# Performance work log

Measured on AMD Instinct MI355X. Metric: run time of the kernel, lower is better.

## Reference

```python
import jax, jax.numpy as jnp
import numpy as np
from jax import lax

B, D, L = 32, 256, 4096
Q, H, T = D // 4, D // 2, 3 * D // 4


def setup_inputs() -> dict:
    key = jax.random.key(0)
    ks = iter(jax.random.split(key, 64))

    def nrm(shape, s=0.02):
        return jax.random.normal(next(ks), shape, jnp.float32) * s

    inp = {"x": jax.random.normal(next(ks), (B, D, L), jnp.float32)}

    def pw(name, o, c):  # pointwise conv: weight [O,C], bias [O]
        inp[name + "_w"] = nrm((o, c))
        inp[name + "_b"] = jnp.zeros((o,), jnp.float32)

    def dw(name, c, k):  # depthwise conv: weight [C,1,K], bias [C]
        inp[name + "_w"] = nrm((c, 1, k))
        inp[name + "_b"] = jnp.zeros((c,), jnp.float32)

    inp["ln1_w"] = jnp.ones((D,), jnp.float32); inp["ln1_b"] = jnp.zeros((D,), jnp.float32)
    pw("a1p", Q, Q); dw("a1d", Q, 7)
    pw("v1", Q, Q); pw("v11", Q, Q); pw("v12", Q, Q)
    dw("c31", Q, 3)
    inp["ln2_w"] = jnp.ones((H,), jnp.float32); inp["ln2_b"] = jnp.zeros((H,), jnp.float32)
    pw("a2p", H, H); dw("a2d", H, 9)
    pw("v2", H, H); pw("v21", H, H); pw("v22", Q, Q)
    pw("p2", Q, H)
    dw("c32", Q, 3)
    inp["ln3_w"] = jnp.ones((T,), jnp.float32); inp["ln3_b"] = jnp.zeros((T,), jnp.float32)
    pw("a3p", T, T); dw("a3d", T, 11)
    pw("v3", T, T); pw("v31", T, T); pw("v32", Q, Q)
    pw("p3", Q, T)
    dw("c33", Q, 3)
    return inp


def _ln_cf(x, w, b, eps=1e-6):
    # channels_first LayerNorm: normalize over channel dim (axis=1)
    u = jnp.mean(x, axis=1, keepdims=True)
    s = jnp.mean((x - u) ** 2, axis=1, keepdims=True)
    return w[:, None] * (x - u) / jnp.sqrt(s + eps) + b[:, None]


def _pw(x, w, b):
    # 1x1 conv1d: x [B,C,L], w [O,C] -> [B,O,L]
    return jnp.einsum('bcl,oc->bol', x, w) + b[:, None]


def _dw(x, w, b, pad):
    # depthwise conv1d: x [B,C,L], w [C,1,K]
    y = lax.conv_general_dilated(x, w, (1,), [(pad, pad)],
                                 dimension_numbers=('NCH', 'OIH', 'NCH'),
                                 feature_group_count=x.shape[1])
    return y + b[:, None]


def reference(x, ln1_w, ln1_b, a1p_w, a1p_b, a1d_w, a1d_b, v1_w, v1_b,
              v11_w, v11_b, v12_w, v12_b, c31_w, c31_b,
              ln2_w, ln2_b, a2p_w, a2p_b, a2d_w, a2d_b, v2_w, v2_b,
              v21_w, v21_b, v22_w, v22_b, p2_w, p2_b, c32_w, c32_b,
              ln3_w, ln3_b, a3p_w, a3p_b, a3d_w, a3d_b, v3_w, v3_b,
              v31_w, v31_b, v32_w, v32_b, p3_w, p3_b, c33_w, c33_b):
    x = _ln_cf(x, ln1_w, ln1_b)
    xs = jnp.split(x, 4, axis=1)  # 4 chunks of Q channels

    # stage 1
    a = _dw(jax.nn.gelu(_pw(xs[0], a1p_w, a1p_b), approximate=False), a1d_w, a1d_b, 3)
    mul = _pw(a * _pw(xs[0], v1_w, v1_b), v11_w, v11_b)
    x1 = _dw(_pw(xs[1], v12_w, v12_b), c31_w, c31_b, 1) + a
    x1 = jnp.concatenate([x1, mul], axis=1)  # [B,H,L]

    # stage 2
    x1 = _ln_cf(x1, ln2_w, ln2_b)
    a = _dw(jax.nn.gelu(_pw(x1, a2p_w, a2p_b), approximate=False), a2d_w, a2d_b, 4)
    mul = _pw(a * _pw(x1, v2_w, v2_b), v21_w, v21_b)
    x2 = _dw(_pw(xs[2], v22_w, v22_b), c32_w, c32_b, 1) + _pw(a, p2_w, p2_b)
    x2 = jnp.concatenate([x2, mul], axis=1)  # [B,T,L]

    # stage 3
    x2 = _ln_cf(x2, ln3_w, ln3_b)
    a = _dw(jax.nn.gelu(_pw(x2, a3p_w, a3p_b), approximate=False), a3d_w, a3d_b, 5)
    mul = _pw(a * _pw(x2, v3_w, v3_b), v31_w, v31_b)
    x3 = _dw(_pw(xs[3], v32_w, v32_b), c33_w, c33_b, 1) + _pw(a, p3_w, p3_b)
    return jnp.concatenate([x3, mul], axis=1)  # [B,D,L]
```

## Files before the change

kernel.cpp:

```cpp
#include <hip/hip_runtime.h>
#include <cmath>


using u16 = unsigned short;
typedef short shrt8 __attribute__((ext_vector_type(8)));
typedef short shrt4 __attribute__((ext_vector_type(4)));
typedef float f32x4 __attribute__((ext_vector_type(4)));

#define DEVI __device__ __forceinline__

static constexpr int TL   = 64;
static constexpr int EXT  = 88;
static constexpr int RS   = 72;
static constexpr int SLOT = EXT * RS;
static constexpr int NW   = 8;

DEVI u16 f2bf(float f) {
    unsigned u = __float_as_uint(f);
    u += 0x7FFFu + ((u >> 16) & 1u);
    return (u16)(u >> 16);
}
DEVI float bf2f(u16 h) { return __uint_as_float(((unsigned)h) << 16); }

DEVI float gelu_f(float x) {
    const float y  = x * 0.70710678118654752f;
    const float ay = fabsf(y);
    const float t  = __builtin_amdgcn_rcpf(fmaf(0.3275911f, ay, 1.0f));
    float p = 1.061405429f;
    p = fmaf(p, t, -1.453152027f);
    p = fmaf(p, t,  1.421413741f);
    p = fmaf(p, t, -0.284496736f);
    p = fmaf(p, t,  0.254829592f);
    float er = 1.0f - p * t * __expf(-ay * ay);
    er = copysignf(er, y);
    return 0.5f * x * (1.0f + er);
}

struct SL { int a, b, c; };
DEVI int slotOf(SL s, int ch) { return ch < 64 ? s.a : (ch < 128 ? s.b : s.c); }

template<int O, int C, bool GELU, bool TOG, bool INPL>
DEVI void pw_mfma(u16* sh, SL in, SL out, const u16* Wb, const float* bias,
                  int elo, int ehi, int l0,
                  float* outg = nullptr, int bidx = 0, int ochan = 0) {
    constexpr int MR = O / 64;
    constexpr int KT = C / 32;
    constexpr int NT = 3;
    const int lane = threadIdx.x & 63;
    const int wv   = threadIdx.x >> 6;
    const int mw = wv >> 1, nw = wv & 1;
    const int col  = lane & 15;
    const int quad = lane >> 4;
    const int mrow = mw * (MR * 16) + col;
    const int kq   = quad * 8;
    const int crow = mw * (MR * 16) + quad * 4;

    f32x4 acc[MR][NT];
    #pragma unroll
    for (int mi = 0; mi < MR; ++mi) {
        const f32x4 bv = *(const f32x4*)(bias + crow + mi * 16);
        #pragma unroll
        for (int ni = 0; ni < NT; ++ni) acc[mi][ni] = bv;
    }
    bool act[NT]; int bpos[NT];
    #pragma unroll
    for (int ni = 0; ni < NT; ++ni) {
        const int nt = nw * NT + ni;
        act[ni] = (nt * 16 < ehi) && (nt * 16 + 16 > elo);
        int p = nt * 16 + col; if (p > EXT - 1) p = EXT - 1;
        bpos[ni] = p;
    }
    #pragma unroll
    for (int kt = 0; kt < KT; ++kt) {
        shrt8 af[MR];
        #pragma unroll
        for (int mi = 0; mi < MR; ++mi)
            af[mi] = *(const shrt8*)(Wb + (size_t)(mrow + mi * 16) * C + kt * 32 + kq);
        const int k0 = kt * 32;
        const u16* bs = sh + slotOf(in, k0) * SLOT + ((k0 & 63) + kq);
        #pragma unroll
        for (int ni = 0; ni < NT; ++ni) {
            if (!act[ni]) continue;
            const shrt8 bf = *(const shrt8*)(bs + bpos[ni] * RS);
            #pragma unroll
            for (int mi = 0; mi < MR; ++mi)
                acc[mi][ni] = __builtin_amdgcn_mfma_f32_16x16x32_bf16(af[mi], bf, acc[mi][ni], 0, 0, 0);
        }
    }
    if (INPL) __syncthreads();
    #pragma unroll
    for (int ni = 0; ni < NT; ++ni) {
        if (!act[ni]) continue;
        const int e = (nw * NT + ni) * 16 + col;
        if (e < elo || e >= ehi) continue;
        const int l = l0 + e;
        #pragma unroll
        for (int mi = 0; mi < MR; ++mi) {
            f32x4 v = acc[mi][ni];
            if (GELU) { v[0]=gelu_f(v[0]); v[1]=gelu_f(v[1]); v[2]=gelu_f(v[2]); v[3]=gelu_f(v[3]); }
            const int ch = crow + mi * 16;
            if (TOG) {
                float* og = outg + ((size_t)bidx * 256 + ochan + ch) * 4096 + l;
                og[0] = v[0]; og[4096] = v[1]; og[2*4096] = v[2]; og[3*4096] = v[3];
            } else {
                const bool gv = (unsigned)l < 4096u;
                shrt4 pk;
                pk[0] = gv ? (short)f2bf(v[0]) : (short)0;
                pk[1] = gv ? (short)f2bf(v[1]) : (short)0;
                pk[2] = gv ? (short)f2bf(v[2]) : (short)0;
                pk[3] = gv ? (short)f2bf(v[3]) : (short)0;
                *(shrt4*)(sh + slotOf(out, ch) * SLOT + e * RS + (ch & 63)) = pk;
            }
        }
    }
}

template<int C, int K, int PAD, int WIN, bool INPL>
DEVI void dw_mul(u16* sh, SL g, SL ao, SL v, const float* W, const float* bias,
                 int elo, int ehi) {
    const int lane = threadIdx.x & 63;
    const int wv   = threadIdx.x >> 6;
    const int nwin  = (ehi - elo + WIN - 1) / WIN;
    const int tasks = (C / 64) * nwin;
    const bool have = wv < tasks;
    float r[K + WIN - 1];
    float wk[K];
    float bo = 0.f;
    int c = 0, e0 = 0;
    if (have) {
        const int cb = wv / nwin, wi = wv - cb * nwin;
        c = cb * 64 + lane;
        #pragma unroll
        for (int k = 0; k < K; ++k) wk[k] = W[c * K + k];
        bo = bias[c];
        e0 = elo + wi * WIN;
        const u16* si = sh + slotOf(g, c) * SLOT + lane;
        #pragma unroll
        for (int m = 0; m < K + WIN - 1; ++m) {
            int e = e0 - PAD + m; if (e > EXT - 1) e = EXT - 1;
            r[m] = bf2f(si[e * RS]);
        }
    }
    if (INPL) __syncthreads();
    if (have) {
        u16* sa = sh + slotOf(ao, c) * SLOT + lane;
        u16* sv = sh + slotOf(v, c) * SLOT + lane;
        #pragma unroll
        for (int j = 0; j < WIN; ++j) {
            const int e = e0 + j;
            if (e >= ehi) break;
            float acc = bo;
            #pragma unroll
            for (int k = 0; k < K; ++k) acc = fmaf(wk[k], r[j + k], acc);
            sa[e * RS] = f2bf(acc);
            sv[e * RS] = f2bf(acc * bf2f(sv[e * RS]));
        }
    }
}

template<int C, int K, int PAD, bool ADD>
DEVI void dw_ph(u16* sh, SL in, SL add, SL out, const float* W, const float* bias,
                int elo, int ehi, int l0) {
    const int lane = threadIdx.x & 63;
    const int wv   = threadIdx.x >> 6;
    const int nwin = (ehi - elo + 7) >> 3;
    const int tasks = (C / 64) * nwin;
    for (int t = wv; t < tasks; t += NW) {
        const int cb = t / nwin, wi = t - cb * nwin;
        const int c = cb * 64 + lane;
        float wk[K];
        #pragma unroll
        for (int k = 0; k < K; ++k) wk[k] = W[c * K + k];
        const float bo = bias[c];
        const int e0 = elo + wi * 8;
        const u16* si = sh + slotOf(in, c) * SLOT + lane;
        const u16* sa = ADD ? (sh + slotOf(add, c) * SLOT + lane) : nullptr;
        u16* so = sh + slotOf(out, c) * SLOT + lane;
        float r[K + 7];
        #pragma unroll
        for (int m = 0; m < K + 7; ++m) {
            int e = e0 - PAD + m; if (e > EXT - 1) e = EXT - 1;
            r[m] = bf2f(si[e * RS]);
        }
        #pragma unroll
        for (int j = 0; j < 8; ++j) {
            const int e = e0 + j;
            if (e >= ehi) break;
            float acc = bo;
            #pragma unroll
            for (int k = 0; k < K; ++k) acc = fmaf(wk[k], r[j + k], acc);
            if (ADD) acc += bf2f(sa[e * RS]);
            const bool gv = (unsigned)(l0 + e) < 4096u;
            so[e * RS] = gv ? f2bf(acc) : (u16)0;
        }
    }
}

template<int C>
DEVI void ln_ph(u16* sh, SL s, const float* W, const float* B,
                int elo, int ehi, int l0, float* scr, float* mean, float* rstd) {
    constexpr int P = C / 64;
    const int tid = threadIdx.x;
    const int nP = ehi - elo;
    if (tid < nP * P) {
        const int e = elo + tid / P;
        const int part = tid - (tid / P) * P;
        const u16* row = sh + slotOf(s, part * 64) * SLOT + e * RS;
        float sm = 0.f, sq = 0.f;
        #pragma unroll
        for (int j = 0; j < 8; ++j) {
            shrt8 v = *(const shrt8*)(row + j * 8);
            #pragma unroll
            for (int i = 0; i < 8; ++i) { float f = bf2f((u16)v[i]); sm += f; sq += f * f; }
        }
        scr[tid * 2] = sm; scr[tid * 2 + 1] = sq;
    }
    __syncthreads();
    if (tid < nP) {
        float sm = 0.f, sq = 0.f;
        for (int p = 0; p < P; ++p) { sm += scr[(tid * P + p) * 2]; sq += scr[(tid * P + p) * 2 + 1]; }
        const float mu = sm * (1.0f / C);
        const float va = sq * (1.0f / C) - mu * mu;
        mean[elo + tid] = mu; rstd[elo + tid] = rsqrtf(va + 1e-6f);
    }
    __syncthreads();
    const int nC8 = C / 8, total = nP * nC8;
    for (int t = tid; t < total; t += 512) {
        const int e  = elo + t / nC8;
        const int c0 = (t - (t / nC8) * nC8) * 8;
        const float mu = mean[e], rs = rstd[e];
        const bool gv = (unsigned)(l0 + e) < 4096u;
        u16* p = sh + slotOf(s, c0) * SLOT + e * RS + (c0 & 63);
        shrt8 v = *(const shrt8*)p, o;
        const f32x4 w0 = *(const f32x4*)(W + c0), w1 = *(const f32x4*)(W + c0 + 4);
        const f32x4 b0 = *(const f32x4*)(B + c0), b1 = *(const f32x4*)(B + c0 + 4);
        #pragma unroll
        for (int i = 0; i < 4; ++i) {
            float f = (bf2f((u16)v[i]) - mu) * rs * w0[i] + b0[i];
            o[i] = gv ? (short)f2bf(f) : (short)0;
        }
        #pragma unroll
        for (int i = 0; i < 4; ++i) {
            float f = (bf2f((u16)v[4 + i]) - mu) * rs * w1[i] + b1[i];
            o[4 + i] = gv ? (short)f2bf(f) : (short)0;
        }
        *(shrt8*)p = o;
    }
}

DEVI void norm_load(u16* sh, int slot, const float* xg, int b, int cbase,
                    const float* lnw, const float* lnb,
                    const float* mean, const float* rstd,
                    int elo, int ehi, int l0) {
    const int lane = threadIdx.x & 63;
    const int wv   = threadIdx.x >> 6;
    #pragma unroll
    for (int j = 0; j < 8; ++j) {
        const int o = wv + NW * j;
        const float* p = xg + ((size_t)b * 256 + cbase + o) * 4096;
        const float wo = lnw[cbase + o], bo = lnb[cbase + o];
        u16* r = sh + slot * SLOT + o;
        #pragma unroll
        for (int part = 0; part < 2; ++part) {
            const int e = elo + lane + part * 64;
            if (e < ehi) {
                const int l = l0 + e;
                const bool gv = (unsigned)l < 4096u;
                float v = gv ? p[l] : 0.f;
                v = (v - mean[e]) * rstd[e] * wo + bo;
                r[e * RS] = gv ? f2bf(v) : (u16)0;
            }
        }
    }
}

DEVI void dw3_glob(u16* sh, int inSlot, int addSlot, const float* W, const float* B,
                   float* outg, int b, int l0) {
    const int tid = threadIdx.x;
    #pragma unroll
    for (int k = 0; k < 8; ++k) {
        const int idx = tid + k * 512;
        const int c   = idx >> 6;
        const int e   = 12 + (idx & 63);
        const u16* si = sh + inSlot * SLOT + c;
        float acc = B[c];
        acc = fmaf(W[c * 3 + 0], bf2f(si[(e - 1) * RS]), acc);
        acc = fmaf(W[c * 3 + 1], bf2f(si[e * RS]), acc);
        acc = fmaf(W[c * 3 + 2], bf2f(si[(e + 1) * RS]), acc);
        acc += bf2f(sh[addSlot * SLOT + e * RS + c]);
        outg[((size_t)b * 256 + c) * 4096 + (l0 + e)] = acc;
    }
}


enum {
    I_X = 0, I_LN1W, I_LN1B, I_A1PW, I_A1PB, I_A1DW, I_A1DB, I_V1W, I_V1B,
    I_V11W, I_V11B, I_V12W, I_V12B, I_C31W, I_C31B,
    I_LN2W, I_LN2B, I_A2PW, I_A2PB, I_A2DW, I_A2DB, I_V2W, I_V2B,
    I_V21W, I_V21B, I_V22W, I_V22B, I_P2W, I_P2B, I_C32W, I_C32B,
    I_LN3W, I_LN3B, I_A3PW, I_A3PB, I_A3DW, I_A3DB, I_V3W, I_V3B,
    I_V31W, I_V31B, I_V32W, I_V32B, I_P3W, I_P3B, I_C33W, I_C33B
};
enum { W_A1P = 0, W_V1, W_V11, W_V12, W_A2P, W_V2, W_V21, W_V22, W_P2,
       W_A3P, W_V3, W_V31, W_V32, W_P3, W_N };

struct KArgs { const float* p[47]; const u16* w[W_N]; const float* stats; float* out; };
struct CvtArgs { const float* src[W_N]; u16* dst; int off[W_N + 1]; };

__global__ __launch_bounds__(256) void cvt_kernel(CvtArgs a) {
    const int i = blockIdx.x * 256 + threadIdx.x;
    if (i >= a.off[W_N]) return;
    int s = 0;
    while (i >= a.off[s + 1]) ++s;
    a.dst[i] = f2bf(a.src[s][i - a.off[s]]);
}

__global__ __launch_bounds__(256) void ln1pre_kernel(const float* x, float* stats) {
    const int b = blockIdx.x >> 4;
    const int l = ((blockIdx.x & 15) << 8) + threadIdx.x;
    const float* p = x + (size_t)b * 256 * 4096 + l;
    float sm = 0.f, sq = 0.f;
    #pragma unroll 4
    for (int c = 0; c < 256; ++c) {
        const float v = p[(size_t)c * 4096];
        sm += v; sq += v * v;
    }
    const float mu = sm * (1.0f / 256.0f);
    const float va = sq * (1.0f / 256.0f) - mu * mu;
    float2 o; o.x = mu; o.y = rsqrtf(va + 1e-6f);
    *(float2*)(stats + 2 * ((size_t)b * 4096 + l)) = o;
}

__global__ __launch_bounds__(512, 4) void convmod_kernel(KArgs a) {
    __shared__ u16 pool[6 * SLOT];
    __shared__ float meanA[EXT], rstdA[EXT], meanB[EXT], rstdB[EXT];
    __shared__ float scr[448];

    const int b    = blockIdx.x >> 6;
    const int tile = blockIdx.x & 63;
    const int l0   = tile * TL - 12;
    const float* xg = a.p[I_X];
    u16* sh = pool;

    if (threadIdx.x < EXT) {
        const int l = l0 + (int)threadIdx.x;
        float mu = 0.f, rs = 1.f;
        if ((unsigned)l < 4096u) {
            const float2 st = *(const float2*)(a.stats + 2 * ((size_t)b * 4096 + l));
            mu = st.x; rs = st.y;
        }
        meanA[threadIdx.x] = mu; rstdA[threadIdx.x] = rs;
    }
    __syncthreads();
    norm_load(sh, 0, xg, b,  0, a.p[I_LN1W], a.p[I_LN1B], meanA, rstdA, 0, EXT, l0);
    norm_load(sh, 1, xg, b, 64, a.p[I_LN1W], a.p[I_LN1B], meanA, rstdA, 0, EXT, l0);
    __syncthreads();
    pw_mfma<64, 64, true,  false, false>(sh, SL{0,-1,-1}, SL{2,-1,-1}, a.w[W_A1P], a.p[I_A1PB], 0, 88, l0);
    pw_mfma<64, 64, false, false, false>(sh, SL{0,-1,-1}, SL{3,-1,-1}, a.w[W_V1],  a.p[I_V1B],  3, 85, l0);
    pw_mfma<64, 64, false, false, false>(sh, SL{1,-1,-1}, SL{4,-1,-1}, a.w[W_V12], a.p[I_V12B], 2, 86, l0);
    __syncthreads();
    dw_mul<64, 7, 3, 16, false>(sh, SL{2,-1,-1}, SL{5,-1,-1}, SL{3,-1,-1}, a.p[I_A1DW], a.p[I_A1DB], 3, 85);
    __syncthreads();
    pw_mfma<64, 64, false, false, false>(sh, SL{3,-1,-1}, SL{2,-1,-1}, a.w[W_V11], a.p[I_V11B], 3, 85, l0);
    dw_ph<64, 3, 1, true>(sh, SL{4,-1,-1}, SL{5,-1,-1}, SL{1,-1,-1}, a.p[I_C31W], a.p[I_C31B], 3, 85, l0);
    __syncthreads();
    ln_ph<128>(sh, SL{1,2,-1}, a.p[I_LN2W], a.p[I_LN2B], 3, 85, l0, scr, meanB, rstdB);
    __syncthreads();
    norm_load(sh, 0, xg, b, 128, a.p[I_LN1W], a.p[I_LN1B], meanA, rstdA, 6, 82, l0);
    pw_mfma<128, 128, true,  false, false>(sh, SL{1,2,-1}, SL{3,4,-1}, a.w[W_A2P], a.p[I_A2PB], 3, 85, l0);
    pw_mfma<128, 128, false, false, true >(sh, SL{1,2,-1}, SL{1,2,-1}, a.w[W_V2],  a.p[I_V2B],  7, 81, l0);
    __syncthreads();
    pw_mfma<64, 64, false, false, false>(sh, SL{0,-1,-1}, SL{5,-1,-1}, a.w[W_V22], a.p[I_V22B], 6, 82, l0);
    dw_mul<128, 9, 4, 19, true>(sh, SL{3,4,-1}, SL{3,4,-1}, SL{1,2,-1}, a.p[I_A2DW], a.p[I_A2DB], 7, 81);
    __syncthreads();
    pw_mfma<64, 128, false, false, false>(sh, SL{3,4,-1}, SL{0,-1,-1}, a.w[W_P2], a.p[I_P2B], 7, 81, l0);
    pw_mfma<128, 128, false, false, true >(sh, SL{1,2,-1}, SL{1,2,-1}, a.w[W_V21], a.p[I_V21B], 7, 81, l0);
    __syncthreads();
    dw_ph<64, 3, 1, true>(sh, SL{5,-1,-1}, SL{0,-1,-1}, SL{3,-1,-1}, a.p[I_C32W], a.p[I_C32B], 7, 81, l0);
    __syncthreads();
    ln_ph<192>(sh, SL{3,1,2}, a.p[I_LN3W], a.p[I_LN3B], 7, 81, l0, scr, meanB, rstdB);
    __syncthreads();
    pw_mfma<192, 192, true,  false, false>(sh, SL{3,1,2}, SL{4,5,0}, a.w[W_A3P], a.p[I_A3PB], 7, 81, l0);
    pw_mfma<192, 192, false, false, true >(sh, SL{3,1,2}, SL{3,1,2}, a.w[W_V3],  a.p[I_V3B],  12, 76, l0);
    __syncthreads();
    dw_mul<192, 11, 5, 32, true>(sh, SL{4,5,0}, SL{4,5,0}, SL{3,1,2}, a.p[I_A3DW], a.p[I_A3DB], 12, 76);
    __syncthreads();
    pw_mfma<192, 192, false, true,  false>(sh, SL{3,1,2}, SL{-1,-1,-1}, a.w[W_V31], a.p[I_V31B], 12, 76, l0, a.out, b, 64);
    pw_mfma<64, 192, false, false, true >(sh, SL{4,5,0}, SL{4,-1,-1}, a.w[W_P3],  a.p[I_P3B],  12, 76, l0);
    norm_load(sh, 5, xg, b, 192, a.p[I_LN1W], a.p[I_LN1B], meanA, rstdA, 11, 77, l0);
    __syncthreads();
    pw_mfma<64, 64, false, false, false>(sh, SL{5,-1,-1}, SL{0,-1,-1}, a.w[W_V32], a.p[I_V32B], 11, 77, l0);
    __syncthreads();
    dw3_glob(sh, 0, 4, a.p[I_C33W], a.p[I_C33B], a.out, b, l0);
}

extern "C" void kernel_launch(void* const* d_in, const int* in_sizes, int n_in,
                              void* d_out, int out_size, void* d_ws, size_t ws_size,
                              hipStream_t stream) {
    (void)in_sizes; (void)n_in; (void)out_size; (void)ws_size;
    static const int widx[W_N] = { I_A1PW, I_V1W, I_V11W, I_V12W, I_A2PW, I_V2W,
                                   I_V21W, I_V22W, I_P2W, I_A3PW, I_V3W, I_V31W,
                                   I_V32W, I_P3W };
    static const int wsz[W_N]  = { 4096, 4096, 4096, 4096, 16384, 16384, 16384,
                                   4096, 8192, 36864, 36864, 36864, 4096, 12288 };
    CvtArgs ca; KArgs ka;
    int off = 0;
    for (int i = 0; i < W_N; ++i) {
        ca.src[i] = (const float*)d_in[widx[i]];
        ca.off[i] = off;
        off += wsz[i];
    }
    ca.off[W_N] = off;
    ca.dst = (u16*)d_ws;
    for (int i = 0; i < 47; ++i) ka.p[i] = (const float*)d_in[i];
    for (int i = 0; i < W_N; ++i) ka.w[i] = (const u16*)d_ws + ca.off[i];
    const size_t stats_off = ((size_t)off * sizeof(u16) + 255) & ~(size_t)255;
    float* stats = (float*)((char*)d_ws + stats_off);
    ka.stats = stats;
    ka.out = (float*)d_out;

    cvt_kernel<<<dim3((off + 255) / 256), dim3(256), 0, stream>>>(ca);
    ln1pre_kernel<<<dim3(32 * 16), dim3(256), 0, stream>>>((const float*)d_in[I_X], stats);
    convmod_kernel<<<dim3(32 * 64), dim3(512), 0, stream>>>(ka);
}
```

Before: 691.8 us.

## Double sequence tile to 128 with 1024 threads and fuse paired pointwise GEMMs

Each block now covers a 128-position tile (152 with halo) using 16 waves instead of 64 positions with 8 waves. This cuts the redundant halo recompute across the cascaded depthwise stages from 24/64 to 24/128. The gelu-path and value-path pointwise convolutions that read the same input are merged into one MFMA pass with a split output, which reuses the input fragments and removes some barriers. In exchange, shared memory per block roughly doubles and the thread count doubles, which lowers occupancy, and the merged GEMMs widen the register tile.

```diff
diff --git a/kernel.cpp b/kernel.cpp
--- a/kernel.cpp
+++ b/kernel.cpp
@@ -9,11 +9,12 @@
 
 #define DEVI __device__ __forceinline__
 
-static constexpr int TL   = 64;
-static constexpr int EXT  = 88;
+static constexpr int TL   = 128;
+static constexpr int EXT  = 152;
 static constexpr int RS   = 72;
 static constexpr int SLOT = EXT * RS;
-static constexpr int NW   = 8;
+static constexpr int NW   = 16;
+static constexpr int NTHR = 1024;
 
 DEVI u16 f2bf(float f) {
     unsigned u = __float_as_uint(f);
@@ -39,8 +40,9 @@
 struct SL { int a, b, c; };
 DEVI int slotOf(SL s, int ch) { return ch < 64 ? s.a : (ch < 128 ? s.b : s.c); }
 
-template<int O, int C, bool GELU, bool TOG, bool INPL>
-DEVI void pw_mfma(u16* sh, SL in, SL out, const u16* Wb, const float* bias,
+template<int O, int C, int OSPLIT, bool GELU, bool TOG, bool INPL>
+DEVI void pw_mfma(u16* sh, SL in, SL outA, SL outB, const u16* Wb,
+                  const float* biasA, const float* biasB,
                   int elo, int ehi, int l0,
                   float* outg = nullptr, int bidx = 0, int ochan = 0) {
     constexpr int MR = O / 64;
@@ -48,7 +50,7 @@
     constexpr int NT = 3;
     const int lane = threadIdx.x & 63;
     const int wv   = threadIdx.x >> 6;
-    const int mw = wv >> 1, nw = wv & 1;
+    const int mw = wv >> 2, nw = wv & 3;
     const int col  = lane & 15;
     const int quad = lane >> 4;
     const int mrow = mw * (MR * 16) + col;
@@ -58,14 +60,17 @@
     f32x4 acc[MR][NT];
     #pragma unroll
     for (int mi = 0; mi < MR; ++mi) {
-        const f32x4 bv = *(const f32x4*)(bias + crow + mi * 16);
+        const int ch = crow + mi * 16;
+        const float* bp = (OSPLIT < O && ch >= OSPLIT) ? (biasB + (ch - OSPLIT))
+                                                       : (biasA + ch);
+        const f32x4 bv = *(const f32x4*)bp;
         #pragma unroll
         for (int ni = 0; ni < NT; ++ni) acc[mi][ni] = bv;
     }
     bool act[NT]; int bpos[NT];
     #pragma unroll
     for (int ni = 0; ni < NT; ++ni) {
-        const int nt = nw * NT + ni;
+        const int nt = nw + 4 * ni;
         act[ni] = (nt * 16 < ehi) && (nt * 16 + 16 > elo);
         int p = nt * 16 + col; if (p > EXT - 1) p = EXT - 1;
         bpos[ni] = p;
@@ -91,25 +96,28 @@
     #pragma unroll
     for (int ni = 0; ni < NT; ++ni) {
         if (!act[ni]) continue;
-        const int e = (nw * NT + ni) * 16 + col;
+        const int e = (nw + 4 * ni) * 16 + col;
         if (e < elo || e >= ehi) continue;
         const int l = l0 + e;
         #pragma unroll
         for (int mi = 0; mi < MR; ++mi) {
             f32x4 v = acc[mi][ni];
-            if (GELU) { v[0]=gelu_f(v[0]); v[1]=gelu_f(v[1]); v[2]=gelu_f(v[2]); v[3]=gelu_f(v[3]); }
             const int ch = crow + mi * 16;
+            const bool isA = !(OSPLIT < O) || (ch < OSPLIT);
+            if (GELU && isA) { v[0]=gelu_f(v[0]); v[1]=gelu_f(v[1]); v[2]=gelu_f(v[2]); v[3]=gelu_f(v[3]); }
             if (TOG) {
                 float* og = outg + ((size_t)bidx * 256 + ochan + ch) * 4096 + l;
                 og[0] = v[0]; og[4096] = v[1]; og[2*4096] = v[2]; og[3*4096] = v[3];
             } else {
+                const int cl = isA ? ch : ch - OSPLIT;
+                const SL  os = isA ? outA : outB;
                 const bool gv = (unsigned)l < 4096u;
                 shrt4 pk;
                 pk[0] = gv ? (short)f2bf(v[0]) : (short)0;
                 pk[1] = gv ? (short)f2bf(v[1]) : (short)0;
                 pk[2] = gv ? (short)f2bf(v[2]) : (short)0;
                 pk[3] = gv ? (short)f2bf(v[3]) : (short)0;
-                *(shrt4*)(sh + slotOf(out, ch) * SLOT + e * RS + (ch & 63)) = pk;
+                *(shrt4*)(sh + slotOf(os, cl) * SLOT + e * RS + (cl & 63)) = pk;
             }
         }
     }
@@ -158,12 +166,12 @@
     }
 }
 
-template<int C, int K, int PAD, bool ADD>
+template<int C, int K, int PAD, int WIN, bool ADD>
 DEVI void dw_ph(u16* sh, SL in, SL add, SL out, const float* W, const float* bias,
                 int elo, int ehi, int l0) {
     const int lane = threadIdx.x & 63;
     const int wv   = threadIdx.x >> 6;
-    const int nwin = (ehi - elo + 7) >> 3;
+    const int nwin = (ehi - elo + WIN - 1) / WIN;
     const int tasks = (C / 64) * nwin;
     for (int t = wv; t < tasks; t += NW) {
         const int cb = t / nwin, wi = t - cb * nwin;
@@ -172,18 +180,18 @@
         #pragma unroll
         for (int k = 0; k < K; ++k) wk[k] = W[c * K + k];
         const float bo = bias[c];
-        const int e0 = elo + wi * 8;
+        const int e0 = elo + wi * WIN;
         const u16* si = sh + slotOf(in, c) * SLOT + lane;
         const u16* sa = ADD ? (sh + slotOf(add, c) * SLOT + lane) : nullptr;
         u16* so = sh + slotOf(out, c) * SLOT + lane;
-        float r[K + 7];
-        #pragma unroll
-        for (int m = 0; m < K + 7; ++m) {
+        float r[K + WIN - 1];
+        #pragma unroll
+        for (int m = 0; m < K + WIN - 1; ++m) {
             int e = e0 - PAD + m; if (e > EXT - 1) e = EXT - 1;
             r[m] = bf2f(si[e * RS]);
         }
         #pragma unroll
-        for (int j = 0; j < 8; ++j) {
+        for (int j = 0; j < WIN; ++j) {
             const int e = e0 + j;
             if (e >= ehi) break;
             float acc = bo;
@@ -225,7 +233,7 @@
     }
     __syncthreads();
     const int nC8 = C / 8, total = nP * nC8;
-    for (int t = tid; t < total; t += 512) {
+    for (int t = tid; t < total; t += NTHR) {
         const int e  = elo + t / nC8;
         const int c0 = (t - (t / nC8) * nC8) * 8;
         const float mu = mean[e], rs = rstd[e];
@@ -255,13 +263,13 @@
     const int lane = threadIdx.x & 63;
     const int wv   = threadIdx.x >> 6;
     #pragma unroll
-    for (int j = 0; j < 8; ++j) {
+    for (int j = 0; j < 4; ++j) {
         const int o = wv + NW * j;
         const float* p = xg + ((size_t)b * 256 + cbase + o) * 4096;
         const float wo = lnw[cbase + o], bo = lnb[cbase + o];
         u16* r = sh + slot * SLOT + o;
         #pragma unroll
-        for (int part = 0; part < 2; ++part) {
+        for (int part = 0; part < 3; ++part) {
             const int e = elo + lane + part * 64;
             if (e < ehi) {
                 const int l = l0 + e;
@@ -279,9 +287,9 @@
     const int tid = threadIdx.x;
     #pragma unroll
     for (int k = 0; k < 8; ++k) {
-        const int idx = tid + k * 512;
-        const int c   = idx >> 6;
-        const int e   = 12 + (idx & 63);
+        const int idx = tid + k * NTHR;
+        const int c   = idx >> 7;
+        const int e   = 12 + (idx & 127);
         const u16* si = sh + inSlot * SLOT + c;
         float acc = B[c];
         acc = fmaf(W[c * 3 + 0], bf2f(si[(e - 1) * RS]), acc);
@@ -331,13 +339,13 @@
     *(float2*)(stats + 2 * ((size_t)b * 4096 + l)) = o;
 }
 
-__global__ __launch_bounds__(512, 4) void convmod_kernel(KArgs a) {
+__global__ __launch_bounds__(NTHR, 4) void convmod_kernel(KArgs a) {
     __shared__ u16 pool[6 * SLOT];
     __shared__ float meanA[EXT], rstdA[EXT], meanB[EXT], rstdB[EXT];
-    __shared__ float scr[448];
-
-    const int b    = blockIdx.x >> 6;
-    const int tile = blockIdx.x & 63;
+    __shared__ float scr[828];
+
+    const int b    = blockIdx.x >> 5;
+    const int tile = blockIdx.x & 31;
     const int l0   = tile * TL - 12;
     const float* xg = a.p[I_X];
     u16* sh = pool;
@@ -355,41 +363,49 @@
     norm_load(sh, 0, xg, b,  0, a.p[I_LN1W], a.p[I_LN1B], meanA, rstdA, 0, EXT, l0);
     norm_load(sh, 1, xg, b, 64, a.p[I_LN1W], a.p[I_LN1B], meanA, rstdA, 0, EXT, l0);
     __syncthreads();
-    pw_mfma<64, 64, true,  false, false>(sh, SL{0,-1,-1}, SL{2,-1,-1}, a.w[W_A1P], a.p[I_A1PB], 0, 88, l0);
-    pw_mfma<64, 64, false, false, false>(sh, SL{0,-1,-1}, SL{3,-1,-1}, a.w[W_V1],  a.p[I_V1B],  3, 85, l0);
-    pw_mfma<64, 64, false, false, false>(sh, SL{1,-1,-1}, SL{4,-1,-1}, a.w[W_V12], a.p[I_V12B], 2, 86, l0);
-    __syncthreads();
-    dw_mul<64, 7, 3, 16, false>(sh, SL{2,-1,-1}, SL{5,-1,-1}, SL{3,-1,-1}, a.p[I_A1DW], a.p[I_A1DB], 3, 85);
-    __syncthreads();
-    pw_mfma<64, 64, false, false, false>(sh, SL{3,-1,-1}, SL{2,-1,-1}, a.w[W_V11], a.p[I_V11B], 3, 85, l0);
-    dw_ph<64, 3, 1, true>(sh, SL{4,-1,-1}, SL{5,-1,-1}, SL{1,-1,-1}, a.p[I_C31W], a.p[I_C31B], 3, 85, l0);
-    __syncthreads();
-    ln_ph<128>(sh, SL{1,2,-1}, a.p[I_LN2W], a.p[I_LN2B], 3, 85, l0, scr, meanB, rstdB);
-    __syncthreads();
-    norm_load(sh, 0, xg, b, 128, a.p[I_LN1W], a.p[I_LN1B], meanA, rstdA, 6, 82, l0);
-    pw_mfma<128, 128, true,  false, false>(sh, SL{1,2,-1}, SL{3,4,-1}, a.w[W_A2P], a.p[I_A2PB], 3, 85, l0);
-    pw_mfma<128, 128, false, false, true >(sh, SL{1,2,-1}, SL{1,2,-1}, a.w[W_V2],  a.p[I_V2B],  7, 81, l0);
-    __syncthreads();
-    pw_mfma<64, 64, false, false, false>(sh, SL{0,-1,-1}, SL{5,-1,-1}, a.w[W_V22], a.p[I_V22B], 6, 82, l0);
-    dw_mul<128, 9, 4, 19, true>(sh, SL{3,4,-1}, SL{3,4,-1}, SL{1,2,-1}, a.p[I_A2DW], a.p[I_A2DB], 7, 81);
-    __syncthreads();
-    pw_mfma<64, 128, false, false, false>(sh, SL{3,4,-1}, SL{0,-1,-1}, a.w[W_P2], a.p[I_P2B], 7, 81, l0);
-    pw_mfma<128, 128, false, false, true >(sh, SL{1,2,-1}, SL{1,2,-1}, a.w[W_V21], a.p[I_V21B], 7, 81, l0);
-    __syncthreads();
-    dw_ph<64, 3, 1, true>(sh, SL{5,-1,-1}, SL{0,-1,-1}, SL{3,-1,-1}, a.p[I_C32W], a.p[I_C32B], 7, 81, l0);
-    __syncthreads();
-    ln_ph<192>(sh, SL{3,1,2}, a.p[I_LN3W], a.p[I_LN3B], 7, 81, l0, scr, meanB, rstdB);
-    __syncthreads();
-    pw_mfma<192, 192, true,  false, false>(sh, SL{3,1,2}, SL{4,5,0}, a.w[W_A3P], a.p[I_A3PB], 7, 81, l0);
-    pw_mfma<192, 192, false, false, true >(sh, SL{3,1,2}, SL{3,1,2}, a.w[W_V3],  a.p[I_V3B],  12, 76, l0);
-    __syncthreads();
-    dw_mul<192, 11, 5, 32, true>(sh, SL{4,5,0}, SL{4,5,0}, SL{3,1,2}, a.p[I_A3DW], a.p[I_A3DB], 12, 76);
-    __syncthreads();
-    pw_mfma<192, 192, false, true,  false>(sh, SL{3,1,2}, SL{-1,-1,-1}, a.w[W_V31], a.p[I_V31B], 12, 76, l0, a.out, b, 64);
-    pw_mfma<64, 192, false, false, true >(sh, SL{4,5,0}, SL{4,-1,-1}, a.w[W_P3],  a.p[I_P3B],  12, 76, l0);
-    norm_load(sh, 5, xg, b, 192, a.p[I_LN1W], a.p[I_LN1B], meanA, rstdA, 11, 77, l0);
-    __syncthreads();
-    pw_mfma<64, 64, false, false, false>(sh, SL{5,-1,-1}, SL{0,-1,-1}, a.w[W_V32], a.p[I_V32B], 11, 77, l0);
+    pw_mfma<128, 64, 64, true, false, false>(sh, SL{0,-1,-1}, SL{2,-1,-1}, SL{3,-1,-1},
+        a.w[W_A1P], a.p[I_A1PB], a.p[I_V1B], 0, 152, l0);
+    pw_mfma<64, 64, 64, false, false, false>(sh, SL{1,-1,-1}, SL{4,-1,-1}, SL{4,-1,-1},
+        a.w[W_V12], a.p[I_V12B], a.p[I_V12B], 2, 150, l0);
+    __syncthreads();
+    dw_mul<64, 7, 3, 10, false>(sh, SL{2,-1,-1}, SL{5,-1,-1}, SL{3,-1,-1}, a.p[I_A1DW], a.p[I_A1DB], 3, 149);
+    __syncthreads();
+    pw_mfma<64, 64, 64, false, false, false>(sh, SL{3,-1,-1}, SL{2,-1,-1}, SL{2,-1,-1},
+        a.w[W_V11], a.p[I_V11B], a.p[I_V11B], 3, 149, l0);
+    dw_ph<64, 3, 1, 10, true>(sh, SL{4,-1,-1}, SL{5,-1,-1}, SL{1,-1,-1}, a.p[I_C31W], a.p[I_C31B], 3, 149, l0);
+    __syncthreads();
+    ln_ph<128>(sh, SL{1,2,-1}, a.p[I_LN2W], a.p[I_LN2B], 3, 149, l0, scr, meanB, rstdB);
+    __syncthreads();
+    norm_load(sh, 0, xg, b, 128, a.p[I_LN1W], a.p[I_LN1B], meanA, rstdA, 6, 146, l0);
+    pw_mfma<256, 128, 128, true, false, true>(sh, SL{1,2,-1}, SL{3,4,-1}, SL{1,2,-1},
+        a.w[W_A2P], a.p[I_A2PB], a.p[I_V2B], 3, 149, l0);
+    __syncthreads();
+    pw_mfma<64, 64, 64, false, false, false>(sh, SL{0,-1,-1}, SL{5,-1,-1}, SL{5,-1,-1},
+        a.w[W_V22], a.p[I_V22B], a.p[I_V22B], 6, 146, l0);
+    dw_mul<128, 9, 4, 18, true>(sh, SL{3,4,-1}, SL{3,4,-1}, SL{1,2,-1}, a.p[I_A2DW], a.p[I_A2DB], 7, 145);
+    __syncthreads();
+    pw_mfma<64, 128, 64, false, false, false>(sh, SL{3,4,-1}, SL{0,-1,-1}, SL{0,-1,-1},
+        a.w[W_P2], a.p[I_P2B], a.p[I_P2B], 7, 145, l0);
+    pw_mfma<128, 128, 128, false, false, true>(sh, SL{1,2,-1}, SL{1,2,-1}, SL{1,2,-1},
+        a.w[W_V21], a.p[I_V21B], a.p[I_V21B], 7, 145, l0);
+    __syncthreads();
+    dw_ph<64, 3, 1, 10, true>(sh, SL{5,-1,-1}, SL{0,-1,-1}, SL{3,-1,-1}, a.p[I_C32W], a.p[I_C32B], 7, 145, l0);
+    __syncthreads();
+    ln_ph<192>(sh, SL{3,1,2}, a.p[I_LN3W], a.p[I_LN3B], 7, 145, l0, scr, meanB, rstdB);
+    __syncthreads();
+    pw_mfma<384, 192, 192, true, false, true>(sh, SL{3,1,2}, SL{4,5,0}, SL{3,1,2},
+        a.w[W_A3P], a.p[I_A3PB], a.p[I_V3B], 7, 145, l0);
+    __syncthreads();
+    dw_mul<192, 11, 5, 26, true>(sh, SL{4,5,0}, SL{4,5,0}, SL{3,1,2}, a.p[I_A3DW], a.p[I_A3DB], 12, 140);
+    __syncthreads();
+    pw_mfma<192, 192, 192, false, true, false>(sh, SL{3,1,2}, SL{-1,-1,-1}, SL{-1,-1,-1},
+        a.w[W_V31], a.p[I_V31B], a.p[I_V31B], 12, 140, l0, a.out, b, 64);
+    pw_mfma<64, 192, 64, false, false, true>(sh, SL{4,5,0}, SL{4,-1,-1}, SL{4,-1,-1},
+        a.w[W_P3], a.p[I_P3B], a.p[I_P3B], 12, 140, l0);
+    norm_load(sh, 5, xg, b, 192, a.p[I_LN1W], a.p[I_LN1B], meanA, rstdA, 11, 141, l0);
+    __syncthreads();
+    pw_mfma<64, 64, 64, false, false, false>(sh, SL{5,-1,-1}, SL{0,-1,-1}, SL{0,-1,-1},
+        a.w[W_V32], a.p[I_V32B], a.p[I_V32B], 11, 141, l0);
     __syncthreads();
     dw3_glob(sh, 0, 4, a.p[I_C33W], a.p[I_C33B], a.out, b, l0);
 }
@@ -421,5 +437,5 @@
 
     cvt_kernel<<<dim3((off + 255) / 256), dim3(256), 0, stream>>>(ca);
     ln1pre_kernel<<<dim3(32 * 16), dim3(256), 0, stream>>>((const float*)d_in[I_X], stats);
-    convmod_kernel<<<dim3(32 * 64), dim3(512), 0, stream>>>(ka);
-}
+    convmod_kernel<<<dim3(32 * 32), dim3(NTHR), 0, stream>>>(ka);
+}
```

Measured after the change: 824.9 us. 19.2% more time.

## Fold LayerNorm affine into pointwise weights and merge sibling projections into one MFMA pass

Applied to the files above, without the earlier changes.

Drops the in-place normalize pass of LN2 and LN3. The LN scale is folded into the bf16 weights at conversion time, and the mean/rstd correction plus bias is applied in the GEMM epilogue using per-channel u/v vectors built by a new small kernel. The a*p and v projections that share an input now run as one stacked MFMA GEMM, as do a1p and v1, which removes redundant B-fragment loads and a barrier or two. The depthwise window sizes are also retuned. The cost is an extra kernel launch and more epilogue arithmetic. The mean-subtraction correction computed from bf16-rounded weights may lose precision.

```diff
diff --git a/kernel.cpp b/kernel.cpp
--- a/kernel.cpp
+++ b/kernel.cpp
@@ -14,6 +14,7 @@
 static constexpr int RS   = 72;
 static constexpr int SLOT = EXT * RS;
 static constexpr int NW   = 8;
+static constexpr int NTHR = 512;
 
 DEVI u16 f2bf(float f) {
     unsigned u = __float_as_uint(f);
@@ -39,9 +40,12 @@
 struct SL { int a, b, c; };
 DEVI int slotOf(SL s, int ch) { return ch < 64 ? s.a : (ch < 128 ? s.b : s.c); }
 
-template<int O, int C, bool GELU, bool TOG, bool INPL>
-DEVI void pw_mfma(u16* sh, SL in, SL out, const u16* Wb, const float* bias,
+template<int O, int C, int OSPLIT, bool GELU, bool TOG, bool INPL, bool LNF>
+DEVI void pw_mfma(u16* sh, SL in, SL outA, SL outB, const u16* Wb,
+                  const float* biasA, const float* biasB,
                   int elo, int ehi, int l0,
+                  const float* uv = nullptr, const float* rsA = nullptr,
+                  const float* mrsA = nullptr,
                   float* outg = nullptr, int bidx = 0, int ochan = 0) {
     constexpr int MR = O / 64;
     constexpr int KT = C / 32;
@@ -58,7 +62,14 @@
     f32x4 acc[MR][NT];
     #pragma unroll
     for (int mi = 0; mi < MR; ++mi) {
-        const f32x4 bv = *(const f32x4*)(bias + crow + mi * 16);
+        f32x4 bv;
+        if (LNF) { bv[0] = 0.f; bv[1] = 0.f; bv[2] = 0.f; bv[3] = 0.f; }
+        else {
+            const int ch = crow + mi * 16;
+            const float* bp = (OSPLIT < O && ch >= OSPLIT) ? (biasB + (ch - OSPLIT))
+                                                           : (biasA + ch);
+            bv = *(const f32x4*)bp;
+        }
         #pragma unroll
         for (int ni = 0; ni < NT; ++ni) acc[mi][ni] = bv;
     }
@@ -88,28 +99,49 @@
         }
     }
     if (INPL) __syncthreads();
+    float rsv[NT], mrsv[NT];
+    if (LNF) {
+        #pragma unroll
+        for (int ni = 0; ni < NT; ++ni) {
+            rsv[ni]  = rsA[bpos[ni]];
+            mrsv[ni] = mrsA[bpos[ni]];
+        }
+    }
     #pragma unroll
-    for (int ni = 0; ni < NT; ++ni) {
-        if (!act[ni]) continue;
-        const int e = (nw * NT + ni) * 16 + col;
-        if (e < elo || e >= ehi) continue;
-        const int l = l0 + e;
-        #pragma unroll
-        for (int mi = 0; mi < MR; ++mi) {
+    for (int mi = 0; mi < MR; ++mi) {
+        const int ch = crow + mi * 16;
+        const bool isA = !(OSPLIT < O) || (ch < OSPLIT);
+        f32x4 u4, v4;
+        if (LNF) {
+            u4 = *(const f32x4*)(uv + ch);
+            v4 = *(const f32x4*)(uv + O + ch);
+        }
+        #pragma unroll
+        for (int ni = 0; ni < NT; ++ni) {
+            if (!act[ni]) continue;
+            const int e = (nw * NT + ni) * 16 + col;
+            if (e < elo || e >= ehi) continue;
+            const int l = l0 + e;
             f32x4 v = acc[mi][ni];
-            if (GELU) { v[0]=gelu_f(v[0]); v[1]=gelu_f(v[1]); v[2]=gelu_f(v[2]); v[3]=gelu_f(v[3]); }
-            const int ch = crow + mi * 16;
+            if (LNF) {
+                #pragma unroll
+                for (int i = 0; i < 4; ++i)
+                    v[i] = fmaf(rsv[ni], v[i], fmaf(-mrsv[ni], v4[i], u4[i]));
+            }
+            if (GELU && isA) { v[0]=gelu_f(v[0]); v[1]=gelu_f(v[1]); v[2]=gelu_f(v[2]); v[3]=gelu_f(v[3]); }
             if (TOG) {
                 float* og = outg + ((size_t)bidx * 256 + ochan + ch) * 4096 + l;
                 og[0] = v[0]; og[4096] = v[1]; og[2*4096] = v[2]; og[3*4096] = v[3];
             } else {
+                const int cl = isA ? ch : ch - OSPLIT;
+                const SL  os = isA ? outA : outB;
                 const bool gv = (unsigned)l < 4096u;
                 shrt4 pk;
                 pk[0] = gv ? (short)f2bf(v[0]) : (short)0;
                 pk[1] = gv ? (short)f2bf(v[1]) : (short)0;
                 pk[2] = gv ? (short)f2bf(v[2]) : (short)0;
                 pk[3] = gv ? (short)f2bf(v[3]) : (short)0;
-                *(shrt4*)(sh + slotOf(out, ch) * SLOT + e * RS + (ch & 63)) = pk;
+                *(shrt4*)(sh + slotOf(os, cl) * SLOT + e * RS + (cl & 63)) = pk;
             }
         }
     }
@@ -158,12 +190,12 @@
     }
 }
 
-template<int C, int K, int PAD, bool ADD>
+template<int C, int K, int PAD, int WIN, bool ADD>
 DEVI void dw_ph(u16* sh, SL in, SL add, SL out, const float* W, const float* bias,
                 int elo, int ehi, int l0) {
     const int lane = threadIdx.x & 63;
     const int wv   = threadIdx.x >> 6;
-    const int nwin = (ehi - elo + 7) >> 3;
+    const int nwin = (ehi - elo + WIN - 1) / WIN;
     const int tasks = (C / 64) * nwin;
     for (int t = wv; t < tasks; t += NW) {
         const int cb = t / nwin, wi = t - cb * nwin;
@@ -172,18 +204,18 @@
         #pragma unroll
         for (int k = 0; k < K; ++k) wk[k] = W[c * K + k];
         const float bo = bias[c];
-        const int e0 = elo + wi * 8;
+        const int e0 = elo + wi * WIN;
         const u16* si = sh + slotOf(in, c) * SLOT + lane;
         const u16* sa = ADD ? (sh + slotOf(add, c) * SLOT + lane) : nullptr;
         u16* so = sh + slotOf(out, c) * SLOT + lane;
-        float r[K + 7];
-        #pragma unroll
-        for (int m = 0; m < K + 7; ++m) {
+        float r[K + WIN - 1];
+        #pragma unroll
+        for (int m = 0; m < K + WIN - 1; ++m) {
             int e = e0 - PAD + m; if (e > EXT - 1) e = EXT - 1;
             r[m] = bf2f(si[e * RS]);
         }
         #pragma unroll
-        for (int j = 0; j < 8; ++j) {
+        for (int j = 0; j < WIN; ++j) {
             const int e = e0 + j;
             if (e >= ehi) break;
             float acc = bo;
@@ -197,8 +229,8 @@
 }
 
 template<int C>
-DEVI void ln_ph(u16* sh, SL s, const float* W, const float* B,
-                int elo, int ehi, int l0, float* scr, float* mean, float* rstd) {
+DEVI void ln_stats(u16* sh, SL s, int elo, int ehi, float* scr,
+                   float* muRS, float* rs) {
     constexpr int P = C / 64;
     const int tid = threadIdx.x;
     const int nP = ehi - elo;
@@ -221,30 +253,8 @@
         for (int p = 0; p < P; ++p) { sm += scr[(tid * P + p) * 2]; sq += scr[(tid * P + p) * 2 + 1]; }
         const float mu = sm * (1.0f / C);
         const float va = sq * (1.0f / C) - mu * mu;
-        mean[elo + tid] = mu; rstd[elo + tid] = rsqrtf(va + 1e-6f);
-    }
-    __syncthreads();
-    const int nC8 = C / 8, total = nP * nC8;
-    for (int t = tid; t < total; t += 512) {
-        const int e  = elo + t / nC8;
-        const int c0 = (t - (t / nC8) * nC8) * 8;
-        const float mu = mean[e], rs = rstd[e];
-        const bool gv = (unsigned)(l0 + e) < 4096u;
-        u16* p = sh + slotOf(s, c0) * SLOT + e * RS + (c0 & 63);
-        shrt8 v = *(const shrt8*)p, o;
-        const f32x4 w0 = *(const f32x4*)(W + c0), w1 = *(const f32x4*)(W + c0 + 4);
-        const f32x4 b0 = *(const f32x4*)(B + c0), b1 = *(const f32x4*)(B + c0 + 4);
-        #pragma unroll
-        for (int i = 0; i < 4; ++i) {
-            float f = (bf2f((u16)v[i]) - mu) * rs * w0[i] + b0[i];
-            o[i] = gv ? (short)f2bf(f) : (short)0;
-        }
-        #pragma unroll
-        for (int i = 0; i < 4; ++i) {
-            float f = (bf2f((u16)v[4 + i]) - mu) * rs * w1[i] + b1[i];
-            o[4 + i] = gv ? (short)f2bf(f) : (short)0;
-        }
-        *(shrt8*)p = o;
+        const float r = rsqrtf(va + 1e-6f);
+        rs[elo + tid] = r; muRS[elo + tid] = mu * r;
     }
 }
 
@@ -279,7 +289,7 @@
     const int tid = threadIdx.x;
     #pragma unroll
     for (int k = 0; k < 8; ++k) {
-        const int idx = tid + k * 512;
+        const int idx = tid + k * NTHR;
         const int c   = idx >> 6;
         const int e   = 12 + (idx & 63);
         const u16* si = sh + inSlot * SLOT + c;
@@ -304,15 +314,54 @@
 enum { W_A1P = 0, W_V1, W_V11, W_V12, W_A2P, W_V2, W_V21, W_V22, W_P2,
        W_A3P, W_V3, W_V31, W_V32, W_P3, W_N };
 
-struct KArgs { const float* p[47]; const u16* w[W_N]; const float* stats; float* out; };
-struct CvtArgs { const float* src[W_N]; u16* dst; int off[W_N + 1]; };
+struct KArgs {
+    const float* p[47]; const u16* w[W_N]; const float* stats;
+    const float* uv2; const float* uv3; float* out;
+};
+struct CvtArgs {
+    const float* src[W_N]; const float* scl[W_N]; u16* dst;
+    int off[W_N + 1]; int cdim[W_N];
+};
+struct UVArgs {
+    const float *w2a, *w2b, *b2a, *b2b, *ln2b;
+    const float *w3a, *w3b, *b3a, *b3b, *ln3b;
+    const u16 *f2, *f3;
+    float *uv2, *uv3;
+};
 
 __global__ __launch_bounds__(256) void cvt_kernel(CvtArgs a) {
     const int i = blockIdx.x * 256 + threadIdx.x;
     if (i >= a.off[W_N]) return;
     int s = 0;
     while (i >= a.off[s + 1]) ++s;
-    a.dst[i] = f2bf(a.src[s][i - a.off[s]]);
+    const int j = i - a.off[s];
+    float v = a.src[s][j];
+    if (a.scl[s]) {
+        const int cd = a.cdim[s];
+        v *= a.scl[s][j - (j / cd) * cd];
+    }
+    a.dst[i] = f2bf(v);
+}
+
+__global__ __launch_bounds__(128) void uv_kernel(UVArgs a) {
+    const int t = blockIdx.x * 128 + threadIdx.x;
+    if (t < 256) {
+        const int o = t;
+        const float* row = o < 128 ? a.w2a + (size_t)o * 128 : a.w2b + (size_t)(o - 128) * 128;
+        float u = o < 128 ? a.b2a[o] : a.b2b[o - 128];
+        float v = 0.f;
+        const u16* fr = a.f2 + (size_t)o * 128;
+        for (int c = 0; c < 128; ++c) { u += row[c] * a.ln2b[c]; v += bf2f(fr[c]); }
+        a.uv2[o] = u; a.uv2[256 + o] = v;
+    } else if (t < 640) {
+        const int o = t - 256;
+        const float* row = o < 192 ? a.w3a + (size_t)o * 192 : a.w3b + (size_t)(o - 192) * 192;
+        float u = o < 192 ? a.b3a[o] : a.b3b[o - 192];
+        float v = 0.f;
+        const u16* fr = a.f3 + (size_t)o * 192;
+        for (int c = 0; c < 192; ++c) { u += row[c] * a.ln3b[c]; v += bf2f(fr[c]); }
+        a.uv3[o] = u; a.uv3[384 + o] = v;
+    }
 }
 
 __global__ __launch_bounds__(256) void ln1pre_kernel(const float* x, float* stats) {
@@ -331,9 +380,9 @@
     *(float2*)(stats + 2 * ((size_t)b * 4096 + l)) = o;
 }
 
-__global__ __launch_bounds__(512, 4) void convmod_kernel(KArgs a) {
+__global__ __launch_bounds__(NTHR, 4) void convmod_kernel(KArgs a) {
     __shared__ u16 pool[6 * SLOT];
-    __shared__ float meanA[EXT], rstdA[EXT], meanB[EXT], rstdB[EXT];
+    __shared__ float meanA[EXT], rstdA[EXT], muRSB[EXT], rsB[EXT];
     __shared__ float scr[448];
 
     const int b    = blockIdx.x >> 6;
@@ -355,41 +404,50 @@
     norm_load(sh, 0, xg, b,  0, a.p[I_LN1W], a.p[I_LN1B], meanA, rstdA, 0, EXT, l0);
     norm_load(sh, 1, xg, b, 64, a.p[I_LN1W], a.p[I_LN1B], meanA, rstdA, 0, EXT, l0);
     __syncthreads();
-    pw_mfma<64, 64, true,  false, false>(sh, SL{0,-1,-1}, SL{2,-1,-1}, a.w[W_A1P], a.p[I_A1PB], 0, 88, l0);
-    pw_mfma<64, 64, false, false, false>(sh, SL{0,-1,-1}, SL{3,-1,-1}, a.w[W_V1],  a.p[I_V1B],  3, 85, l0);
-    pw_mfma<64, 64, false, false, false>(sh, SL{1,-1,-1}, SL{4,-1,-1}, a.w[W_V12], a.p[I_V12B], 2, 86, l0);
+    pw_mfma<128, 64, 64, true, false, false, false>(sh, SL{0,-1,-1}, SL{2,-1,-1}, SL{3,-1,-1},
+        a.w[W_A1P], a.p[I_A1PB], a.p[I_V1B], 0, 88, l0);
+    pw_mfma<64, 64, 64, false, false, false, false>(sh, SL{1,-1,-1}, SL{4,-1,-1}, SL{4,-1,-1},
+        a.w[W_V12], a.p[I_V12B], a.p[I_V12B], 2, 86, l0);
     __syncthreads();
     dw_mul<64, 7, 3, 16, false>(sh, SL{2,-1,-1}, SL{5,-1,-1}, SL{3,-1,-1}, a.p[I_A1DW], a.p[I_A1DB], 3, 85);
     __syncthreads();
-    pw_mfma<64, 64, false, false, false>(sh, SL{3,-1,-1}, SL{2,-1,-1}, a.w[W_V11], a.p[I_V11B], 3, 85, l0);
-    dw_ph<64, 3, 1, true>(sh, SL{4,-1,-1}, SL{5,-1,-1}, SL{1,-1,-1}, a.p[I_C31W], a.p[I_C31B], 3, 85, l0);
-    __syncthreads();
-    ln_ph<128>(sh, SL{1,2,-1}, a.p[I_LN2W], a.p[I_LN2B], 3, 85, l0, scr, meanB, rstdB);
+    pw_mfma<64, 64, 64, false, false, false, false>(sh, SL{3,-1,-1}, SL{2,-1,-1}, SL{2,-1,-1},
+        a.w[W_V11], a.p[I_V11B], a.p[I_V11B], 3, 85, l0);
+    dw_ph<64, 3, 1, 11, true>(sh, SL{4,-1,-1}, SL{5,-1,-1}, SL{1,-1,-1}, a.p[I_C31W], a.p[I_C31B], 3, 85, l0);
+    __syncthreads();
+    ln_stats<128>(sh, SL{1,2,-1}, 3, 85, scr, muRSB, rsB);
     __syncthreads();
     norm_load(sh, 0, xg, b, 128, a.p[I_LN1W], a.p[I_LN1B], meanA, rstdA, 6, 82, l0);
-    pw_mfma<128, 128, true,  false, false>(sh, SL{1,2,-1}, SL{3,4,-1}, a.w[W_A2P], a.p[I_A2PB], 3, 85, l0);
-    pw_mfma<128, 128, false, false, true >(sh, SL{1,2,-1}, SL{1,2,-1}, a.w[W_V2],  a.p[I_V2B],  7, 81, l0);
-    __syncthreads();
-    pw_mfma<64, 64, false, false, false>(sh, SL{0,-1,-1}, SL{5,-1,-1}, a.w[W_V22], a.p[I_V22B], 6, 82, l0);
+    pw_mfma<256, 128, 128, true, false, true, true>(sh, SL{1,2,-1}, SL{3,4,-1}, SL{1,2,-1},
+        a.w[W_A2P], nullptr, nullptr, 3, 85, l0, a.uv2, rsB, muRSB);
+    __syncthreads();
+    pw_mfma<64, 64, 64, false, false, false, false>(sh, SL{0,-1,-1}, SL{5,-1,-1}, SL{5,-1,-1},
+        a.w[W_V22], a.p[I_V22B], a.p[I_V22B], 6, 82, l0);
     dw_mul<128, 9, 4, 19, true>(sh, SL{3,4,-1}, SL{3,4,-1}, SL{1,2,-1}, a.p[I_A2DW], a.p[I_A2DB], 7, 81);
     __syncthreads();
-    pw_mfma<64, 128, false, false, false>(sh, SL{3,4,-1}, SL{0,-1,-1}, a.w[W_P2], a.p[I_P2B], 7, 81, l0);
-    pw_mfma<128, 128, false, false, true >(sh, SL{1,2,-1}, SL{1,2,-1}, a.w[W_V21], a.p[I_V21B], 7, 81, l0);
-    __syncthreads();
-    dw_ph<64, 3, 1, true>(sh, SL{5,-1,-1}, SL{0,-1,-1}, SL{3,-1,-1}, a.p[I_C32W], a.p[I_C32B], 7, 81, l0);
-    __syncthreads();
-    ln_ph<192>(sh, SL{3,1,2}, a.p[I_LN3W], a.p[I_LN3B], 7, 81, l0, scr, meanB, rstdB);
-    __syncthreads();
-    pw_mfma<192, 192, true,  false, false>(sh, SL{3,1,2}, SL{4,5,0}, a.w[W_A3P], a.p[I_A3PB], 7, 81, l0);
-    pw_mfma<192, 192, false, false, true >(sh, SL{3,1,2}, SL{3,1,2}, a.w[W_V3],  a.p[I_V3B],  12, 76, l0);
+    pw_mfma<64, 128, 64, false, false, false, false>(sh, SL{3,4,-1}, SL{0,-1,-1}, SL{0,-1,-1},
+        a.w[W_P2], a.p[I_P2B], a.p[I_P2B], 7, 81, l0);
+    pw_mfma<128, 128, 128, false, false, true, false>(sh, SL{1,2,-1}, SL{1,2,-1}, SL{1,2,-1},
+        a.w[W_V21], a.p[I_V21B], a.p[I_V21B], 7, 81, l0);
+    __syncthreads();
+    dw_ph<64, 3, 1, 10, true>(sh, SL{5,-1,-1}, SL{0,-1,-1}, SL{3,-1,-1}, a.p[I_C32W], a.p[I_C32B], 7, 81, l0);
+    __syncthreads();
+    ln_stats<192>(sh, SL{3,1,2}, 7, 81, scr, muRSB, rsB);
+    __syncthreads();
+    pw_mfma<384, 192, 192, true, false, true, true>(sh, SL{3,1,2}, SL{4,5,0}, SL{3,1,2},
+        a.w[W_A3P], nullptr, nullptr, 7, 81, l0, a.uv3, rsB, muRSB);
     __syncthreads();
     dw_mul<192, 11, 5, 32, true>(sh, SL{4,5,0}, SL{4,5,0}, SL{3,1,2}, a.p[I_A3DW], a.p[I_A3DB], 12, 76);
     __syncthreads();
-    pw_mfma<192, 192, false, true,  false>(sh, SL{3,1,2}, SL{-1,-1,-1}, a.w[W_V31], a.p[I_V31B], 12, 76, l0, a.out, b, 64);
-    pw_mfma<64, 192, false, false, true >(sh, SL{4,5,0}, SL{4,-1,-1}, a.w[W_P3],  a.p[I_P3B],  12, 76, l0);
+    pw_mfma<192, 192, 192, false, true, false, false>(sh, SL{3,1,2}, SL{-1,-1,-1}, SL{-1,-1,-1},
+        a.w[W_V31], a.p[I_V31B], a.p[I_V31B], 12, 76, l0,
+        nullptr, nullptr, nullptr, a.out, b, 64);
+    pw_mfma<64, 192, 64, false, false, true, false>(sh, SL{4,5,0}, SL{4,-1,-1}, SL{4,-1,-1},
+        a.w[W_P3], a.p[I_P3B], a.p[I_P3B], 12, 76, l0);
     norm_load(sh, 5, xg, b, 192, a.p[I_LN1W], a.p[I_LN1B], meanA, rstdA, 11, 77, l0);
     __syncthreads();
-    pw_mfma<64, 64, false, false, false>(sh, SL{5,-1,-1}, SL{0,-1,-1}, a.w[W_V32], a.p[I_V32B], 11, 77, l0);
+    pw_mfma<64, 64, 64, false, false, false, false>(sh, SL{5,-1,-1}, SL{0,-1,-1}, SL{0,-1,-1},
+        a.w[W_V32], a.p[I_V32B], a.p[I_V32B], 11, 77, l0);
     __syncthreads();
     dw3_glob(sh, 0, 4, a.p[I_C33W], a.p[I_C33B], a.out, b, l0);
 }
@@ -403,23 +461,45 @@
                                    I_V32W, I_P3W };
     static const int wsz[W_N]  = { 4096, 4096, 4096, 4096, 16384, 16384, 16384,
                                    4096, 8192, 36864, 36864, 36864, 4096, 12288 };
+    static const int wcd[W_N]  = { 64, 64, 64, 64, 128, 128, 128, 64, 128,
+                                   192, 192, 192, 64, 192 };
     CvtArgs ca; KArgs ka;
     int off = 0;
     for (int i = 0; i < W_N; ++i) {
-        ca.src[i] = (const float*)d_in[widx[i]];
-        ca.off[i] = off;
+        ca.src[i]  = (const float*)d_in[widx[i]];
+        ca.scl[i]  = nullptr;
+        ca.cdim[i] = wcd[i];
+        ca.off[i]  = off;
         off += wsz[i];
     }
+    ca.scl[W_A2P] = (const float*)d_in[I_LN2W];
+    ca.scl[W_V2]  = (const float*)d_in[I_LN2W];
+    ca.scl[W_A3P] = (const float*)d_in[I_LN3W];
+    ca.scl[W_V3]  = (const float*)d_in[I_LN3W];
     ca.off[W_N] = off;
     ca.dst = (u16*)d_ws;
     for (int i = 0; i < 47; ++i) ka.p[i] = (const float*)d_in[i];
     for (int i = 0; i < W_N; ++i) ka.w[i] = (const u16*)d_ws + ca.off[i];
     const size_t stats_off = ((size_t)off * sizeof(u16) + 255) & ~(size_t)255;
     float* stats = (float*)((char*)d_ws + stats_off);
-    ka.stats = stats;
+    float* uv2   = (float*)((char*)d_ws + stats_off + (size_t)32 * 4096 * 2 * 4);
+    float* uv3   = uv2 + 512;
+    ka.stats = stats; ka.uv2 = uv2; ka.uv3 = uv3;
     ka.out = (float*)d_out;
 
+    UVArgs ua;
+    ua.w2a = (const float*)d_in[I_A2PW]; ua.w2b = (const float*)d_in[I_V2W];
+    ua.b2a = (const float*)d_in[I_A2PB]; ua.b2b = (const float*)d_in[I_V2B];
+    ua.ln2b = (const float*)d_in[I_LN2B];
+    ua.w3a = (const float*)d_in[I_A3PW]; ua.w3b = (const float*)d_in[I_V3W];
+    ua.b3a = (const float*)d_in[I_A3PB]; ua.b3b = (const float*)d_in[I_V3B];
+    ua.ln3b = (const float*)d_in[I_LN3B];
+    ua.f2 = (const u16*)d_ws + ca.off[W_A2P];
+    ua.f3 = (const u16*)d_ws + ca.off[W_A3P];
+    ua.uv2 = uv2; ua.uv3 = uv3;
+
     cvt_kernel<<<dim3((off + 255) / 256), dim3(256), 0, stream>>>(ca);
+    uv_kernel<<<dim3(5), dim3(128), 0, stream>>>(ua);
     ln1pre_kernel<<<dim3(32 * 16), dim3(256), 0, stream>>>((const float*)d_in[I_X], stats);
-    convmod_kernel<<<dim3(32 * 64), dim3(512), 0, stream>>>(ka);
-}
+    convmod_kernel<<<dim3(32 * 64), dim3(NTHR), 0, stream>>>(ka);
+}
```

Result: slower. 825.1 us (+19.3%).
